# Kernel optimization log

Measured on AMD Instinct MI355X. Metric: run time of the kernel, lower is better.

Reference implementation:

```python
import jax, jax.numpy as jnp
import numpy as np

NUM_HEADS = 12
MASK_BIAS = -1000.0


def setup_inputs() -> dict:
    key = jax.random.key(0)
    k1, k2, k3, k4 = jax.random.split(key, 4)
    B, N, C = 2, 2048, 768
    x = jax.random.normal(k1, (B, N, C), dtype=jnp.float32)
    # key-padding mask: 1.0 = masked-out position (gets -1000 bias), 0.0 = visible
    mask = jax.random.randint(k2, (B, N), 0, 2).astype(jnp.float32)
    qkv_w = jax.random.normal(k3, (3 * C, C), dtype=jnp.float32) * (1.0 / np.sqrt(C))
    proj_w = jax.random.normal(k4, (C, C), dtype=jnp.float32) * (1.0 / np.sqrt(C))
    proj_b = jnp.zeros((C,), dtype=jnp.float32)
    return {"x": x, "mask": mask, "qkv_w": qkv_w, "proj_w": proj_w, "proj_b": proj_b}


def reference(x, mask, qkv_w, proj_w, proj_b):
    B, N, C = x.shape
    H = NUM_HEADS
    D = C // H
    scale = D ** (-0.5)
    # qkv: Linear without bias -> [B, N, 3C] -> [3, B, H, N, D]
    qkv = (x @ qkv_w.T).reshape(B, N, 3, H, D).transpose(2, 0, 3, 1, 4)
    q, k, v = qkv[0], qkv[1], qkv[2]
    # scores [B, H, N, N]
    attn = jnp.einsum("bhqd,bhkd->bhqk", q, k) * scale
    attn = attn + mask[:, None, None, :] * MASK_BIAS
    attn = jax.nn.softmax(attn, axis=-1)
    out = jnp.einsum("bhqk,bhkd->bhqd", attn, v)  # [B, H, N, D]
    out = out.transpose(0, 2, 1, 3).reshape(B, N, C)
    return out @ proj_w.T + proj_b
```

## Files before the change

kernel.cpp:

```cpp
#include <hip/hip_runtime.h>

typedef __bf16 bf16_t;
typedef __bf16 bf16x8 __attribute__((ext_vector_type(8)));
typedef float f32x4 __attribute__((ext_vector_type(4)));

#define NUM_B 2
#define NUM_H 12
#define SEQ_N 2048
#define DIM_C 768
#define HEAD_D 64
#define BH_CNT (NUM_B * NUM_H)
#define MTOK (NUM_B * SEQ_N)
#define QSCALE 0.1803368801111137f

#define AS1(p) ((const __attribute__((address_space(1))) void*)(p))
#define AS3(p) ((__attribute__((address_space(3))) void*)(p))

__global__ __launch_bounds__(256) void cvt_kernel(
    const float* __restrict__ s0, const float* __restrict__ s1,
    const float* __restrict__ s2, const float* __restrict__ msk,
    bf16_t* __restrict__ d0, bf16_t* __restrict__ d1, bf16_t* __restrict__ d2,
    bf16_t* __restrict__ dw, int nb0, int nb1, int nb2) {
  const int blk = blockIdx.x;
  const float* src;
  bf16_t* dst;
  size_t off;
  bool isw = false;
  if (blk < nb0) {
    src = s0; dst = d0; off = (size_t)blk * 2048;
  } else if (blk < nb0 + nb1) {
    src = s1; dst = d1; off = (size_t)(blk - nb0) * 2048;
  } else if (blk < nb0 + nb1 + nb2) {
    src = s2; dst = d2; off = (size_t)(blk - nb0 - nb1) * 2048;
  } else {
    src = msk; dst = dw; off = (size_t)(blk - nb0 - nb1 - nb2) * 2048;
    isw = true;
  }
  const size_t i = off + (size_t)threadIdx.x * 8;
  float4 f0 = *reinterpret_cast<const float4*>(&src[i]);
  float4 f1 = *reinterpret_cast<const float4*>(&src[i + 4]);
  if (isw) {
    f0 = {1.0f - f0.x, 1.0f - f0.y, 1.0f - f0.z, 1.0f - f0.w};
    f1 = {1.0f - f1.x, 1.0f - f1.y, 1.0f - f1.z, 1.0f - f1.w};
  }
  union { ushort4 u; bf16_t h[4]; } p0, p1;
  p0.h[0] = (bf16_t)f0.x; p0.h[1] = (bf16_t)f0.y;
  p0.h[2] = (bf16_t)f0.z; p0.h[3] = (bf16_t)f0.w;
  p1.h[0] = (bf16_t)f1.x; p1.h[1] = (bf16_t)f1.y;
  p1.h[2] = (bf16_t)f1.z; p1.h[3] = (bf16_t)f1.w;
  *reinterpret_cast<ushort4*>(&dst[i]) = p0.u;
  *reinterpret_cast<ushort4*>(&dst[i + 4]) = p1.u;
}

template <int EPI>
__global__ __launch_bounds__(256, 4) void gemm_bt_kernel(
    const bf16_t* __restrict__ A, const bf16_t* __restrict__ W,
    const float* __restrict__ bias, const float* __restrict__ mask,
    void* __restrict__ outv) {
  __shared__ __align__(16) bf16_t As[2][64 * 32];
  __shared__ __align__(16) bf16_t Bs[2][128 * 32];

  const int tid = threadIdx.x;
  const int wave = tid >> 6, lane = tid & 63;
  const int quad = lane >> 4, l16 = lane & 15;
  const int m0 = blockIdx.y * 64, n0 = blockIdx.x * 128;
  const int wm = (wave >> 1) * 32, wn = (wave & 1) * 64;

  f32x4 acc[2][4] = {};

  const int srow = tid >> 2;
  const int scol = ((tid & 3) ^ ((tid >> 3) & 3)) * 8;
  const bf16_t* gA = A + (size_t)(m0 + srow) * DIM_C + scol;
  const bf16_t* gB0 = W + (size_t)(n0 + srow) * DIM_C + scol;
  const bf16_t* gB1 = W + (size_t)(n0 + srow + 64) * DIM_C + scol;
  const int lb = wave * 512;

  auto issue = [&](int buf, int k0) {
    __builtin_amdgcn_global_load_lds(AS1(gA + k0), AS3(&As[buf][lb]), 16, 0, 0);
    __builtin_amdgcn_global_load_lds(AS1(gB0 + k0), AS3(&Bs[buf][lb]), 16, 0, 0);
    __builtin_amdgcn_global_load_lds(AS1(gB1 + k0), AS3(&Bs[buf][lb + 2048]), 16, 0, 0);
  };

  issue(0, 0);
  int cur = 0;
  const int sw = (l16 >> 1) & 3;
  for (int step = 0; step < DIM_C / 32; ++step) {
    __syncthreads();
    if (step + 1 < DIM_C / 32) issue(cur ^ 1, (step + 1) * 32);

    bf16x8 aF[2], bF[4];
#pragma unroll
    for (int mi = 0; mi < 2; ++mi)
      aF[mi] = *reinterpret_cast<const bf16x8*>(
          &As[cur][(wm + mi * 16 + l16) * 32 + ((quad ^ sw) * 8)]);
#pragma unroll
    for (int ni = 0; ni < 4; ++ni)
      bF[ni] = *reinterpret_cast<const bf16x8*>(
          &Bs[cur][(wn + ni * 16 + l16) * 32 + ((quad ^ sw) * 8)]);
#pragma unroll
    for (int mi = 0; mi < 2; ++mi)
#pragma unroll
      for (int ni = 0; ni < 4; ++ni)
        acc[mi][ni] = __builtin_amdgcn_mfma_f32_16x16x32_bf16(aF[mi], bF[ni],
                                                              acc[mi][ni], 0, 0, 0);
    cur ^= 1;
  }

#pragma unroll
  for (int mi = 0; mi < 2; ++mi) {
#pragma unroll
    for (int ni = 0; ni < 4; ++ni) {
      const int gmB = m0 + wm + mi * 16 + quad * 4;
      const int gn = n0 + wn + ni * 16 + l16;
      if (EPI == 0) {
        bf16_t* out = (bf16_t*)outv;
        const int which = gn / DIM_C;
        const int rem = gn - which * DIM_C;
        const int h = rem >> 6, d = rem & 63;
        const int b = gmB >> 11, tok0 = gmB & 2047;
        if (which < 2) {
          const float sc = (which == 0) ? QSCALE : 1.0f;
          const size_t base = (size_t)which * ((size_t)BH_CNT * SEQ_N * HEAD_D);
#pragma unroll
          for (int r = 0; r < 4; ++r) {
            out[base + (((size_t)(b * NUM_H + h) * SEQ_N + tok0 + r) * HEAD_D + d)] =
                (bf16_t)(acc[mi][ni][r] * sc);
          }
        } else {
          const size_t base = 2ull * BH_CNT * SEQ_N * HEAD_D;
          float4 mv = *reinterpret_cast<const float4*>(&mask[b * SEQ_N + tok0]);
          union { ushort4 u; bf16_t h4[4]; } pk;
          pk.h4[0] = (bf16_t)(acc[mi][ni][0] * (1.0f - mv.x));
          pk.h4[1] = (bf16_t)(acc[mi][ni][1] * (1.0f - mv.y));
          pk.h4[2] = (bf16_t)(acc[mi][ni][2] * (1.0f - mv.z));
          pk.h4[3] = (bf16_t)(acc[mi][ni][3] * (1.0f - mv.w));
          *reinterpret_cast<ushort4*>(
              &out[base + (((size_t)(b * NUM_H + h) * HEAD_D + d) * SEQ_N + tok0)]) =
              pk.u;
        }
      } else {
        float* out = (float*)outv;
        const float bv = bias[gn];
#pragma unroll
        for (int r = 0; r < 4; ++r) {
          const int gm = gmB + r;
          out[(size_t)gm * DIM_C + gn] = acc[mi][ni][r] + bv;
        }
      }
    }
  }
}

__global__ __launch_bounds__(256, 4) void attn_kernel(
    const bf16_t* __restrict__ q, const bf16_t* __restrict__ k,
    const bf16_t* __restrict__ vt, const bf16_t* __restrict__ wv,
    bf16_t* __restrict__ ctx) {
  __shared__ __align__(16) bf16_t Ks[2][64 * 64];
  __shared__ __align__(16) bf16_t Vs[2][64 * 64];
  __shared__ __align__(16) bf16_t Ps[4][1024];

  const int tid = threadIdx.x;
  const int wave = tid >> 6, lane = tid & 63;
  const int quad = lane >> 4, l16 = lane & 15;
  const int bh = blockIdx.y;
  const int b = bh / NUM_H, h = bh - b * NUM_H;
  const int q0 = blockIdx.x * 64 + wave * 16;

  const bf16_t* qb = q + (size_t)bh * SEQ_N * HEAD_D;
  const bf16_t* kb = k + (size_t)bh * SEQ_N * HEAD_D;
  const bf16_t* vtb = vt + (size_t)bh * HEAD_D * SEQ_N;
  const bf16_t* wb = wv + (size_t)b * SEQ_N;

  bf16x8 qf[2];
#pragma unroll
  for (int ks = 0; ks < 2; ++ks)
    qf[ks] = *reinterpret_cast<const bf16x8*>(
        &qb[(size_t)(q0 + l16) * HEAD_D + ks * 32 + quad * 8]);

  f32x4 acc[4] = {};
  f32x4 acc_l = {};

  const int srow = tid >> 3;
  const int scol = ((tid & 7) ^ ((tid >> 3) & 7)) * 8;
  const bf16_t* gK0 = kb + (size_t)srow * HEAD_D + scol;
  const bf16_t* gK1 = kb + (size_t)(srow + 32) * HEAD_D + scol;
  const bf16_t* gV0 = vtb + (size_t)srow * SEQ_N + scol;
  const bf16_t* gV1 = vtb + (size_t)(srow + 32) * SEQ_N + scol;
  const int lb = wave * 512;

  auto issueKV = [&](int buf, int key0) {
    __builtin_amdgcn_global_load_lds(AS1(gK0 + (size_t)key0 * HEAD_D),
                                     AS3(&Ks[buf][lb]), 16, 0, 0);
    __builtin_amdgcn_global_load_lds(AS1(gK1 + (size_t)key0 * HEAD_D),
                                     AS3(&Ks[buf][lb + 2048]), 16, 0, 0);
    __builtin_amdgcn_global_load_lds(AS1(gV0 + key0), AS3(&Vs[buf][lb]), 16, 0, 0);
    __builtin_amdgcn_global_load_lds(AS1(gV1 + key0), AS3(&Vs[buf][lb + 2048]),
                                     16, 0, 0);
  };

  issueKV(0, 0);
  int cur = 0;
  const int swz = l16 & 7;
  const int psbase = wave * 1024 + l16 * 64;
  for (int key0 = 0; key0 < SEQ_N; key0 += 64) {
    __syncthreads();
    if (key0 + 64 < SEQ_N) issueKV(cur ^ 1, key0 + 64);

    f32x4 s[4];
#pragma unroll
    for (int kt = 0; kt < 4; ++kt) {
      const int row = kt * 16 + l16;
      bf16x8 kf0 = *reinterpret_cast<const bf16x8*>(
          &Ks[cur][row * 64 + ((quad ^ swz) * 8)]);
      bf16x8 kf1 = *reinterpret_cast<const bf16x8*>(
          &Ks[cur][row * 64 + (((4 + quad) ^ swz) * 8)]);
      f32x4 z = {0.0f, 0.0f, 0.0f, 0.0f};
      z = __builtin_amdgcn_mfma_f32_16x16x32_bf16(kf0, qf[0], z, 0, 0, 0);
      s[kt] = __builtin_amdgcn_mfma_f32_16x16x32_bf16(kf1, qf[1], z, 0, 0, 0);
    }

#pragma unroll
    for (int kt = 0; kt < 4; ++kt) {
      union { ushort4 u; bf16_t h4[4]; } pk;
      pk.h4[0] = (bf16_t)exp2f(s[kt][0]);
      pk.h4[1] = (bf16_t)exp2f(s[kt][1]);
      pk.h4[2] = (bf16_t)exp2f(s[kt][2]);
      pk.h4[3] = (bf16_t)exp2f(s[kt][3]);
      const int c = kt * 2 + (quad >> 1);
      *reinterpret_cast<ushort4*>(
          &Ps[0][psbase + ((c ^ swz) << 3) + ((quad & 1) << 2)]) = pk.u;
    }

    bf16x8 pf0 = *reinterpret_cast<const bf16x8*>(
        &Ps[0][psbase + ((quad ^ swz) << 3)]);
    bf16x8 pf1 = *reinterpret_cast<const bf16x8*>(
        &Ps[0][psbase + (((4 + quad) ^ swz) << 3)]);
    bf16x8 wf0 = *reinterpret_cast<const bf16x8*>(&wb[key0 + quad * 8]);
    bf16x8 wf1 = *reinterpret_cast<const bf16x8*>(&wb[key0 + 32 + quad * 8]);
    acc_l = __builtin_amdgcn_mfma_f32_16x16x32_bf16(pf0, wf0, acc_l, 0, 0, 0);
    acc_l = __builtin_amdgcn_mfma_f32_16x16x32_bf16(pf1, wf1, acc_l, 0, 0, 0);

#pragma unroll
    for (int dt = 0; dt < 4; ++dt) {
      const int row = dt * 16 + l16;
      bf16x8 vf0 = *reinterpret_cast<const bf16x8*>(
          &Vs[cur][row * 64 + ((quad ^ swz) * 8)]);
      bf16x8 vf1 = *reinterpret_cast<const bf16x8*>(
          &Vs[cur][row * 64 + (((4 + quad) ^ swz) * 8)]);
      acc[dt] = __builtin_amdgcn_mfma_f32_16x16x32_bf16(pf0, vf0, acc[dt], 0, 0, 0);
      acc[dt] = __builtin_amdgcn_mfma_f32_16x16x32_bf16(pf1, vf1, acc[dt], 0, 0, 0);
    }
    cur ^= 1;
  }

  float rl[4];
#pragma unroll
  for (int r = 0; r < 4; ++r) rl[r] = 1.0f / acc_l[r];
#pragma unroll
  for (int dt = 0; dt < 4; ++dt)
#pragma unroll
    for (int r = 0; r < 4; ++r) {
      const int tok = q0 + quad * 4 + r;
      ctx[((size_t)b * SEQ_N + tok) * DIM_C + h * HEAD_D + dt * 16 + l16] =
          (bf16_t)(acc[dt][r] * rl[r]);
    }
}

extern "C" void kernel_launch(void* const* d_in, const int* in_sizes, int n_in,
                              void* d_out, int out_size, void* d_ws,
                              size_t ws_size, hipStream_t stream) {
  const float* x = (const float*)d_in[0];
  const float* mask = (const float*)d_in[1];
  const float* qkv_w = (const float*)d_in[2];
  const float* proj_w = (const float*)d_in[3];
  const float* proj_b = (const float*)d_in[4];
  float* out = (float*)d_out;

  const size_t nx = (size_t)MTOK * DIM_C;
  const size_t nqw = (size_t)3 * DIM_C * DIM_C;
  const size_t npw = (size_t)DIM_C * DIM_C;
  const size_t nmask = (size_t)NUM_B * SEQ_N;
  const size_t per = (size_t)BH_CNT * SEQ_N * HEAD_D;

  bf16_t* xb = (bf16_t*)d_ws;
  bf16_t* qwb = xb + nx;
  bf16_t* pwb = qwb + nqw;
  bf16_t* wvb = pwb + npw;
  bf16_t* qkv = wvb + nmask;
  bf16_t* ctx = qkv + 3 * per;

  const int nb0 = (int)(nx / 2048), nb1 = (int)(nqw / 2048),
            nb2 = (int)(npw / 2048), nbm = (int)(nmask / 2048);

  cvt_kernel<<<nb0 + nb1 + nb2 + nbm, 256, 0, stream>>>(
      x, qkv_w, proj_w, mask, xb, qwb, pwb, wvb, nb0, nb1, nb2);
  gemm_bt_kernel<0><<<dim3(3 * DIM_C / 128, MTOK / 64), 256, 0, stream>>>(
      xb, qwb, nullptr, mask, qkv);
  attn_kernel<<<dim3(SEQ_N / 64, BH_CNT), 256, 0, stream>>>(
      qkv, qkv + per, qkv + 2 * per, wvb, ctx);
  gemm_bt_kernel<1><<<dim3(DIM_C / 128, MTOK / 64), 256, 0, stream>>>(
      ctx, pwb, proj_b, nullptr, out);
}
```

Measured before the change: 171.2 us.

## Split GEMM into larger-tile QKV kernel and smaller-tile projection kernel

The shared templated GEMM is split into two specialized kernels. The QKV GEMM now uses 128x128 tiles (4x4 MFMA per wave) for more operand reuse, and for the V block it swaps the MFMA operands so accumulators come out transposed for the V^T store. The projection GEMM moves to 64x64 tiles, giving more blocks for better CU fill on the small output. The larger QKV tile raises register and LDS use (occupancy hint lowered to 3), and the V epilogue now writes single bf16 elements strided by token instead of packed 4-wide stores.

Measured after the change: 175.0 us. 1.02x slower.

```diff
diff --git a/kernel.cpp b/kernel.cpp
--- a/kernel.cpp
+++ b/kernel.cpp
@@ -52,31 +52,32 @@
   *reinterpret_cast<ushort4*>(&dst[i + 4]) = p1.u;
 }
 
-template <int EPI>
-__global__ __launch_bounds__(256, 4) void gemm_bt_kernel(
+__global__ __launch_bounds__(256, 3) void gemm_qkv_kernel(
     const bf16_t* __restrict__ A, const bf16_t* __restrict__ W,
-    const float* __restrict__ bias, const float* __restrict__ mask,
-    void* __restrict__ outv) {
-  __shared__ __align__(16) bf16_t As[2][64 * 32];
+    const float* __restrict__ mask, bf16_t* __restrict__ out) {
+  __shared__ __align__(16) bf16_t As[2][128 * 32];
   __shared__ __align__(16) bf16_t Bs[2][128 * 32];
 
   const int tid = threadIdx.x;
   const int wave = tid >> 6, lane = tid & 63;
   const int quad = lane >> 4, l16 = lane & 15;
-  const int m0 = blockIdx.y * 64, n0 = blockIdx.x * 128;
-  const int wm = (wave >> 1) * 32, wn = (wave & 1) * 64;
-
-  f32x4 acc[2][4] = {};
+  const int m0 = blockIdx.y * 128, n0 = blockIdx.x * 128;
+  const int wm = (wave >> 1) * 64, wn = (wave & 1) * 64;
+  const bool vmode = (n0 >= 2 * DIM_C);
+
+  f32x4 acc[4][4] = {};
 
   const int srow = tid >> 2;
   const int scol = ((tid & 3) ^ ((tid >> 3) & 3)) * 8;
-  const bf16_t* gA = A + (size_t)(m0 + srow) * DIM_C + scol;
+  const bf16_t* gA0 = A + (size_t)(m0 + srow) * DIM_C + scol;
+  const bf16_t* gA1 = A + (size_t)(m0 + srow + 64) * DIM_C + scol;
   const bf16_t* gB0 = W + (size_t)(n0 + srow) * DIM_C + scol;
   const bf16_t* gB1 = W + (size_t)(n0 + srow + 64) * DIM_C + scol;
   const int lb = wave * 512;
 
   auto issue = [&](int buf, int k0) {
-    __builtin_amdgcn_global_load_lds(AS1(gA + k0), AS3(&As[buf][lb]), 16, 0, 0);
+    __builtin_amdgcn_global_load_lds(AS1(gA0 + k0), AS3(&As[buf][lb]), 16, 0, 0);
+    __builtin_amdgcn_global_load_lds(AS1(gA1 + k0), AS3(&As[buf][lb + 2048]), 16, 0, 0);
     __builtin_amdgcn_global_load_lds(AS1(gB0 + k0), AS3(&Bs[buf][lb]), 16, 0, 0);
     __builtin_amdgcn_global_load_lds(AS1(gB1 + k0), AS3(&Bs[buf][lb + 2048]), 16, 0, 0);
   };
@@ -88,19 +89,120 @@
     __syncthreads();
     if (step + 1 < DIM_C / 32) issue(cur ^ 1, (step + 1) * 32);
 
-    bf16x8 aF[2], bF[4];
+    bf16x8 aF[4], bF[4];
+#pragma unroll
+    for (int mi = 0; mi < 4; ++mi)
+      aF[mi] = *reinterpret_cast<const bf16x8*>(
+          &As[cur][(wm + mi * 16 + l16) * 32 + ((quad ^ sw) * 8)]);
+#pragma unroll
+    for (int ni = 0; ni < 4; ++ni)
+      bF[ni] = *reinterpret_cast<const bf16x8*>(
+          &Bs[cur][(wn + ni * 16 + l16) * 32 + ((quad ^ sw) * 8)]);
+    if (vmode) {
+#pragma unroll
+      for (int mi = 0; mi < 4; ++mi)
+#pragma unroll
+        for (int ni = 0; ni < 4; ++ni)
+          acc[mi][ni] = __builtin_amdgcn_mfma_f32_16x16x32_bf16(
+              bF[ni], aF[mi], acc[mi][ni], 0, 0, 0);
+    } else {
+#pragma unroll
+      for (int mi = 0; mi < 4; ++mi)
+#pragma unroll
+        for (int ni = 0; ni < 4; ++ni)
+          acc[mi][ni] = __builtin_amdgcn_mfma_f32_16x16x32_bf16(
+              aF[mi], bF[ni], acc[mi][ni], 0, 0, 0);
+    }
+    cur ^= 1;
+  }
+
+  if (!vmode) {
+#pragma unroll
+    for (int mi = 0; mi < 4; ++mi) {
+#pragma unroll
+      for (int ni = 0; ni < 4; ++ni) {
+        const int gmB = m0 + wm + mi * 16 + quad * 4;
+        const int gn = n0 + wn + ni * 16 + l16;
+        const int which = gn / DIM_C;
+        const int rem = gn - which * DIM_C;
+        const int h = rem >> 6, d = rem & 63;
+        const float sc = (which == 0) ? QSCALE : 1.0f;
+        const size_t base = (size_t)which * ((size_t)BH_CNT * SEQ_N * HEAD_D);
+#pragma unroll
+        for (int r = 0; r < 4; ++r) {
+          const int gm = gmB + r;
+          const int b = gm >> 11, tok = gm & 2047;
+          out[base + (((size_t)(b * NUM_H + h) * SEQ_N + tok) * HEAD_D + d)] =
+              (bf16_t)(acc[mi][ni][r] * sc);
+        }
+      }
+    }
+  } else {
+    const size_t base = 2ull * BH_CNT * SEQ_N * HEAD_D;
+#pragma unroll
+    for (int mi = 0; mi < 4; ++mi) {
+      const int tok = m0 + wm + mi * 16 + l16;
+      const float wvf = 1.0f - mask[tok];
+      const int b = tok >> 11, tokm = tok & 2047;
+#pragma unroll
+      for (int ni = 0; ni < 4; ++ni) {
+#pragma unroll
+        for (int r = 0; r < 4; ++r) {
+          const int rowg = n0 - 2 * DIM_C + wn + ni * 16 + quad * 4 + r;
+          const int h = rowg >> 6, d = rowg & 63;
+          out[base + (((size_t)(b * NUM_H + h) * HEAD_D + d) * SEQ_N + tokm)] =
+              (bf16_t)(acc[mi][ni][r] * wvf);
+        }
+      }
+    }
+  }
+}
+
+__global__ __launch_bounds__(256, 4) void gemm_proj_kernel(
+    const bf16_t* __restrict__ A, const bf16_t* __restrict__ W,
+    const float* __restrict__ bias, float* __restrict__ out) {
+  __shared__ __align__(16) bf16_t As[2][64 * 32];
+  __shared__ __align__(16) bf16_t Bs[2][64 * 32];
+
+  const int tid = threadIdx.x;
+  const int wave = tid >> 6, lane = tid & 63;
+  const int quad = lane >> 4, l16 = lane & 15;
+  const int m0 = blockIdx.y * 64, n0 = blockIdx.x * 64;
+  const int wm = (wave >> 1) * 32, wn = (wave & 1) * 32;
+
+  f32x4 acc[2][2] = {};
+
+  const int srow = tid >> 2;
+  const int scol = ((tid & 3) ^ ((tid >> 3) & 3)) * 8;
+  const bf16_t* gA = A + (size_t)(m0 + srow) * DIM_C + scol;
+  const bf16_t* gB = W + (size_t)(n0 + srow) * DIM_C + scol;
+  const int lb = wave * 512;
+
+  auto issue = [&](int buf, int k0) {
+    __builtin_amdgcn_global_load_lds(AS1(gA + k0), AS3(&As[buf][lb]), 16, 0, 0);
+    __builtin_amdgcn_global_load_lds(AS1(gB + k0), AS3(&Bs[buf][lb]), 16, 0, 0);
+  };
+
+  issue(0, 0);
+  int cur = 0;
+  const int sw = (l16 >> 1) & 3;
+  for (int step = 0; step < DIM_C / 32; ++step) {
+    __syncthreads();
+    if (step + 1 < DIM_C / 32) issue(cur ^ 1, (step + 1) * 32);
+
+    bf16x8 aF[2], bF[2];
 #pragma unroll
     for (int mi = 0; mi < 2; ++mi)
       aF[mi] = *reinterpret_cast<const bf16x8*>(
           &As[cur][(wm + mi * 16 + l16) * 32 + ((quad ^ sw) * 8)]);
 #pragma unroll
-    for (int ni = 0; ni < 4; ++ni)
+    for (int ni = 0; ni < 2; ++ni)
       bF[ni] = *reinterpret_cast<const bf16x8*>(
           &Bs[cur][(wn + ni * 16 + l16) * 32 + ((quad ^ sw) * 8)]);
 #pragma unroll
     for (int mi = 0; mi < 2; ++mi)
 #pragma unroll
-      for (int ni = 0; ni < 4; ++ni)
+      for (int ni = 0; ni < 2; ++ni)
         acc[mi][ni] = __builtin_amdgcn_mfma_f32_16x16x32_bf16(aF[mi], bF[ni],
                                                               acc[mi][ni], 0, 0, 0);
     cur ^= 1;
@@ -109,44 +211,13 @@
 #pragma unroll
   for (int mi = 0; mi < 2; ++mi) {
 #pragma unroll
-    for (int ni = 0; ni < 4; ++ni) {
+    for (int ni = 0; ni < 2; ++ni) {
       const int gmB = m0 + wm + mi * 16 + quad * 4;
       const int gn = n0 + wn + ni * 16 + l16;
-      if (EPI == 0) {
-        bf16_t* out = (bf16_t*)outv;
-        const int which = gn / DIM_C;
-        const int rem = gn - which * DIM_C;
-        const int h = rem >> 6, d = rem & 63;
-        const int b = gmB >> 11, tok0 = gmB & 2047;
-        if (which < 2) {
-          const float sc = (which == 0) ? QSCALE : 1.0f;
-          const size_t base = (size_t)which * ((size_t)BH_CNT * SEQ_N * HEAD_D);
-#pragma unroll
-          for (int r = 0; r < 4; ++r) {
-            out[base + (((size_t)(b * NUM_H + h) * SEQ_N + tok0 + r) * HEAD_D + d)] =
-                (bf16_t)(acc[mi][ni][r] * sc);
-          }
-        } else {
-          const size_t base = 2ull * BH_CNT * SEQ_N * HEAD_D;
-          float4 mv = *reinterpret_cast<const float4*>(&mask[b * SEQ_N + tok0]);
-          union { ushort4 u; bf16_t h4[4]; } pk;
-          pk.h4[0] = (bf16_t)(acc[mi][ni][0] * (1.0f - mv.x));
-          pk.h4[1] = (bf16_t)(acc[mi][ni][1] * (1.0f - mv.y));
-          pk.h4[2] = (bf16_t)(acc[mi][ni][2] * (1.0f - mv.z));
-          pk.h4[3] = (bf16_t)(acc[mi][ni][3] * (1.0f - mv.w));
-          *reinterpret_cast<ushort4*>(
-              &out[base + (((size_t)(b * NUM_H + h) * HEAD_D + d) * SEQ_N + tok0)]) =
-              pk.u;
-        }
-      } else {
-        float* out = (float*)outv;
-        const float bv = bias[gn];
-#pragma unroll
-        for (int r = 0; r < 4; ++r) {
-          const int gm = gmB + r;
-          out[(size_t)gm * DIM_C + gn] = acc[mi][ni][r] + bv;
-        }
-      }
+      const float bv = bias[gn];
+#pragma unroll
+      for (int r = 0; r < 4; ++r)
+        out[(size_t)(gmB + r) * DIM_C + gn] = acc[mi][ni][r] + bv;
     }
   }
 }
@@ -294,10 +365,10 @@
 
   cvt_kernel<<<nb0 + nb1 + nb2 + nbm, 256, 0, stream>>>(
       x, qkv_w, proj_w, mask, xb, qwb, pwb, wvb, nb0, nb1, nb2);
-  gemm_bt_kernel<0><<<dim3(3 * DIM_C / 128, MTOK / 64), 256, 0, stream>>>(
-      xb, qwb, nullptr, mask, qkv);
+  gemm_qkv_kernel<<<dim3(3 * DIM_C / 128, MTOK / 128), 256, 0, stream>>>(
+      xb, qwb, mask, qkv);
   attn_kernel<<<dim3(SEQ_N / 64, BH_CNT), 256, 0, stream>>>(
       qkv, qkv + per, qkv + 2 * per, wvb, ctx);
-  gemm_bt_kernel<1><<<dim3(DIM_C / 128, MTOK / 64), 256, 0, stream>>>(
-      ctx, pwb, proj_b, nullptr, out);
-}
+  gemm_proj_kernel<<<dim3(DIM_C / 64, MTOK / 64), 256, 0, stream>>>(
+      ctx, pwb, proj_b, out);
+}
```
